# Kernel optimization log

Hardware: AMD Instinct MI355X
Metric: run time of the kernel (lower is better)

## Reference

```python
import jax, jax.numpy as jnp
import numpy as np

N_HEADS = 16
ROPE_BASE = 10000.0


def _rope_tables(T, Dh, dtype):
    # inv_freq over even indices of head_dim, per RotaryEmbedding
    inv_freq = 1.0 / (ROPE_BASE ** (jnp.arange(0, Dh, 2, dtype=jnp.float32) / Dh))
    freqs = jnp.outer(jnp.arange(T, dtype=jnp.float32), inv_freq)  # [T, Dh/2]
    emb = jnp.concatenate([freqs, freqs], axis=-1)                  # [T, Dh]
    return emb.astype(dtype).reshape(1, 1, T, Dh), None


def _rotate_half(x):
    x1, x2 = jnp.split(x, 2, axis=-1)
    return jnp.concatenate([-x2, x1], axis=-1)


def setup_inputs() -> dict:
    key = jax.random.key(0)
    k1, k2, k3 = jax.random.split(key, 3)
    B, T, C = 2, 2048, 1024
    x = jax.random.normal(k1, (B, T, C), dtype=jnp.float32)
    w_qkv = jax.random.normal(k2, (C, 3 * C), dtype=jnp.float32) * (1.0 / np.sqrt(C))
    w_out = jax.random.normal(k3, (C, C), dtype=jnp.float32) * (1.0 / np.sqrt(C))
    return {"x": x, "w_qkv": w_qkv, "w_out": w_out}


def reference(x, w_qkv, w_out):
    B, T, C = x.shape
    H = N_HEADS
    Dh = C // H
    qkv = x @ w_qkv                                   # [B, T, 3C]
    q, k, v = jnp.split(qkv, 3, axis=-1)
    # [B, T, C] -> [B, H, T, Dh]
    def to_heads(t):
        return t.reshape(B, T, H, Dh).transpose(0, 2, 1, 3)
    q, k, v = to_heads(q), to_heads(k), to_heads(v)

    # RoPE
    emb, _ = _rope_tables(T, Dh, x.dtype)             # [1,1,T,Dh] angle table
    cos, sin = jnp.cos(emb), jnp.sin(emb)
    q = q * cos + _rotate_half(q) * sin
    k = k * cos + _rotate_half(k) * sin

    # causal SDPA (eval mode -> no dropout)
    scale = 1.0 / jnp.sqrt(jnp.asarray(Dh, dtype=x.dtype))
    scores = jnp.einsum('bhqd,bhkd->bhqk', q, k) * scale
    causal_mask = jnp.tril(jnp.ones((T, T), dtype=bool))
    scores = jnp.where(causal_mask, scores, jnp.asarray(-jnp.inf, dtype=scores.dtype))
    attn = jax.nn.softmax(scores, axis=-1)
    out = jnp.einsum('bhqk,bhkd->bhqd', attn, v)      # [B,H,T,Dh]
    out = out.transpose(0, 2, 1, 3).reshape(B, T, C)
    return out @ w_out
```

## Files before the change

kernel.cpp:

```cpp
#include <hip/hip_runtime.h>
#include <stdint.h>


typedef __attribute__((ext_vector_type(8))) __bf16 bf16x8;
typedef __attribute__((ext_vector_type(4))) __bf16 bf16x4;
typedef __attribute__((ext_vector_type(4))) float f32x4;

#define MFMA16(a, b, c) __builtin_amdgcn_mfma_f32_16x16x32_bf16((a), (b), (c), 0, 0, 0)

#define SWAIT_VM0()                                     \
    do {                                                \
        asm volatile("s_waitcnt vmcnt(0)" ::: "memory");\
        __builtin_amdgcn_sched_barrier(0);              \
    } while (0)
#define SWAIT_LGKM0()                                     \
    do {                                                  \
        asm volatile("s_waitcnt lgkmcnt(0)" ::: "memory");\
        __builtin_amdgcn_sched_barrier(0);                \
    } while (0)

__device__ __forceinline__ void gl_lds16(const void* g, void* l) {
    __builtin_amdgcn_global_load_lds(
        (const __attribute__((address_space(1))) void*)g,
        (__attribute__((address_space(3))) void*)l, 16, 0, 0);
}

__device__ __forceinline__ unsigned short f2bf(float f) {
    union { float f; unsigned u; } x; x.f = f;
    unsigned r = x.u + 0x7FFFu + ((x.u >> 16) & 1u);
    return (unsigned short)(r >> 16);
}
__device__ __forceinline__ float bf2f(unsigned short h) {
    union { unsigned u; float f; } x; x.u = ((unsigned)h) << 16;
    return x.f;
}
__device__ __forceinline__ f32x4 fmax4(f32x4 a, f32x4 b) {
    f32x4 r;
#pragma unroll
    for (int i = 0; i < 4; i++) r[i] = fmaxf(a[i], b[i]);
    return r;
}

__global__ void cast_f32_bf16(const float* __restrict__ src,
                              unsigned short* __restrict__ dst, int n4) {
    int i = blockIdx.x * 256 + threadIdx.x;
    if (i >= n4) return;
    float4 v = ((const float4*)src)[i];
    ushort4 o;
    o.x = f2bf(v.x); o.y = f2bf(v.y); o.z = f2bf(v.z); o.w = f2bf(v.w);
    ((ushort4*)dst)[i] = o;
}

__global__ void transpose_cast(const float* __restrict__ src,
                               unsigned short* __restrict__ dst, int K, int N) {
    __shared__ float tile[32][33];
    int n0 = blockIdx.x * 32, k0 = blockIdx.y * 32;
    int r = threadIdx.x >> 5, c = threadIdx.x & 31;
#pragma unroll
    for (int i = 0; i < 4; i++) {
        int kk = r + i * 8;
        tile[kk][c] = src[(size_t)(k0 + kk) * N + n0 + c];
    }
    __syncthreads();
#pragma unroll
    for (int i = 0; i < 4; i++) {
        int nn = r + i * 8;
        dst[(size_t)(n0 + nn) * K + k0 + c] = f2bf(tile[c][nn]);
    }
}

__global__ void rope_tables(float2* __restrict__ cst) {
    int idx = blockIdx.x * 256 + threadIdx.x;
    int t = idx >> 5, d = idx & 31;
    float inv = powf(10000.0f, -(float)(2 * d) / 64.0f);
    float a = (float)t * inv;
    cst[idx] = make_float2(cosf(a), sinf(a));
}

template <int MODE>
__global__ __launch_bounds__(256) void gemm_bt(
    const unsigned short* __restrict__ A,
    const unsigned short* __restrict__ Bt,
    unsigned short* __restrict__ oq,
    unsigned short* __restrict__ ok,
    unsigned short* __restrict__ ovt,
    float* __restrict__ of,
    const float2* __restrict__ cst,
    int M_, int N_, int K_) {
    __shared__ __attribute__((aligned(16))) unsigned short ldsA[128 * 64];
    __shared__ __attribute__((aligned(16))) unsigned short ldsB[128 * 64];
    const int tid = threadIdx.x;
    const int lane = tid & 63, wv = tid >> 6;
    const int wr = wv >> 1, wc = wv & 1;
    const int l15 = lane & 15, lg = lane >> 4;
    const int lrow = lane >> 3, lch = lane & 7;
    const int swz = (lch * 16) ^ (lrow << 4);
    const int m0 = blockIdx.x * 128, n0 = blockIdx.y * 128;
    const char* Ab = (const char*)A;
    const char* Bb = (const char*)Bt;
    const size_t rstride = (size_t)K_ * 2;

    f32x4 acc[4][4] = {};

    const int nkt = K_ >> 6;
    for (int kt = 0; kt < nkt; kt++) {
        if (kt) __syncthreads();
#pragma unroll
        for (int ii = 0; ii < 4; ii++) {
            int r0 = wv * 32 + ii * 8;
            gl_lds16(Ab + (size_t)(m0 + r0 + lrow) * rstride + kt * 128 + swz,
                     (char*)ldsA + r0 * 128);
            gl_lds16(Bb + (size_t)(n0 + r0 + lrow) * rstride + kt * 128 + swz,
                     (char*)ldsB + r0 * 128);
        }
        __syncthreads();
#pragma unroll
        for (int ks = 0; ks < 2; ks++) {
            const int kb = ks * 64 + lg * 16;
            bf16x8 af[4], bfr[4];
#pragma unroll
            for (int mf = 0; mf < 4; mf++) {
                int row = wr * 64 + mf * 16 + l15;
                af[mf] = *(const bf16x8*)((const char*)ldsA + row * 128 +
                                          (kb ^ ((row & 7) << 4)));
            }
#pragma unroll
            for (int nf = 0; nf < 4; nf++) {
                int row = wc * 64 + nf * 16 + l15;
                bfr[nf] = *(const bf16x8*)((const char*)ldsB + row * 128 +
                                           (kb ^ ((row & 7) << 4)));
            }
#pragma unroll
            for (int mf = 0; mf < 4; mf++)
#pragma unroll
                for (int nf = 0; nf < 4; nf++)
                    acc[mf][nf] = MFMA16(af[mf], bfr[nf], acc[mf][nf]);
        }
    }

    if (MODE == 0) {
        const int sblk = n0 >> 10;
        if (sblk == 2) {
#pragma unroll
            for (int mf = 0; mf < 4; mf++)
#pragma unroll
                for (int nf = 0; nf < 4; nf++)
#pragma unroll
                    for (int j = 0; j < 4; j++) {
                        int grow = m0 + wr * 64 + mf * 16 + lg * 4 + j;
                        int gcol = n0 + wc * 64 + nf * 16 + l15;
                        int b = grow >> 11, t = grow & 2047;
                        int c = gcol & 1023;
                        int h = c >> 6, d = c & 63;
                        int hb = b * 16 + h;
                        ovt[((size_t)hb * 64 + d) * 2048 + t] =
                            f2bf(acc[mf][nf][j]);
                    }
        } else {
            const float QSC = 0.125f * 1.44269504f;
            unsigned short* dst = (sblk == 0) ? oq : ok;
#pragma unroll
            for (int mf = 0; mf < 4; mf++)
#pragma unroll
                for (int j = 0; j < 4; j++) {
                    int grow = m0 + wr * 64 + mf * 16 + lg * 4 + j;
                    int b = grow >> 11, t = grow & 2047;
#pragma unroll
                    for (int nf = 0; nf < 2; nf++) {
                        int gcol = n0 + wc * 64 + nf * 16 + l15;
                        int c = gcol & 1023;
                        int h = c >> 6;
                        int d = nf * 16 + l15;
                        int hb = b * 16 + h;
                        float2 csv = cst[t * 32 + d];
                        float x1 = acc[mf][nf][j];
                        float x2 = acc[mf][nf + 2][j];
                        float r1 = x1 * csv.x - x2 * csv.y;
                        float r2 = x2 * csv.x + x1 * csv.y;
                        if (sblk == 0) { r1 *= QSC; r2 *= QSC; }
                        size_t base = ((size_t)hb * 2048 + t) * 64;
                        dst[base + d] = f2bf(r1);
                        dst[base + d + 32] = f2bf(r2);
                    }
                }
        }
    } else {
#pragma unroll
        for (int mf = 0; mf < 4; mf++)
#pragma unroll
            for (int nf = 0; nf < 4; nf++)
#pragma unroll
                for (int j = 0; j < 4; j++) {
                    int grow = m0 + wr * 64 + mf * 16 + lg * 4 + j;
                    int gcol = n0 + wc * 64 + nf * 16 + l15;
                    of[(size_t)grow * N_ + gcol] = acc[mf][nf][j];
                }
    }
}

__global__ __launch_bounds__(256) void attn_fwd(
    const unsigned short* __restrict__ Q,
    const unsigned short* __restrict__ K,
    const unsigned short* __restrict__ Vt,
    unsigned short* __restrict__ O) {
    __shared__ __attribute__((aligned(16))) char ldsKV[4][16384];
    __shared__ __attribute__((aligned(16))) char ldsP[4][2560];
    __shared__ float ml[4][32][2];
    const int tid = threadIdx.x, lane = tid & 63, wv = tid >> 6;
    const int l15 = lane & 15, lg = lane >> 4;
    const int lrow = lane >> 3, lch = lane & 7;
    const int swz = (lch * 16) ^ (lrow << 4);

    const int wg = blockIdx.x;
    const int jt = 63 - (wg >> 5);
    const int bh = (wg & 7) * 4 + ((wg >> 3) & 3);
    const int q0 = jt * 32;
    const int nkt = (jt >> 1) + 1;
    const int lo = (wv * nkt) >> 2;
    const int hi = ((wv + 1) * nkt) >> 2;
    const int b = bh >> 4, h = bh & 15;

    const unsigned short* Qh = Q + (size_t)bh * 2048 * 64;
    const char* Kg = (const char*)(K + (size_t)bh * 2048 * 64);
    const char* Vg = (const char*)(Vt + (size_t)bh * 64 * 2048);
    char* Kb = ldsKV[wv];
    char* Vb = ldsKV[wv] + 8192;
    char* Pb = ldsP[wv];

    bf16x8 qa[2][2];
#pragma unroll
    for (int mf = 0; mf < 2; mf++)
#pragma unroll
        for (int ks = 0; ks < 2; ks++)
            qa[mf][ks] = *(const bf16x8*)(Qh + (size_t)(q0 + mf * 16 + l15) * 64 +
                                          ks * 32 + lg * 8);

    auto stage = [&](int k0) {
        const char* kg = Kg + (size_t)k0 * 128;
        const char* vg = Vg + (size_t)k0 * 2;
#pragma unroll
        for (int ii = 0; ii < 8; ii++) {
            gl_lds16(kg + (ii * 8 + lrow) * 128 + swz, Kb + ii * 1024);
            gl_lds16(vg + (size_t)(ii * 8 + lrow) * 4096 + swz, Vb + ii * 1024);
        }
    };

    f32x4 oacc[2][4] = {};
    float mi[2] = {-1e30f, -1e30f}, li[2] = {0.f, 0.f};

    if (lo < hi) {
        stage(lo * 64);
        for (int kt = lo; kt < hi; kt++) {
            const int k0 = kt * 64;
            SWAIT_VM0();
            bf16x8 kb[2][4], vb[2][4];
#pragma unroll
            for (int ks = 0; ks < 2; ks++)
#pragma unroll
                for (int nf = 0; nf < 4; nf++) {
                    int row = nf * 16 + l15;
                    kb[ks][nf] = *(const bf16x8*)(
                        Kb + row * 128 + ((ks * 64 + lg * 16) ^ ((row & 7) << 4)));
                }
#pragma unroll
            for (int ks = 0; ks < 2; ks++)
#pragma unroll
                for (int df = 0; df < 4; df++) {
                    int row = df * 16 + l15;
                    vb[ks][df] = *(const bf16x8*)(
                        Vb + row * 128 + ((ks * 64 + lg * 16) ^ ((row & 7) << 4)));
                }
            f32x4 s[2][4] = {};
#pragma unroll
            for (int ks = 0; ks < 2; ks++)
#pragma unroll
                for (int mf = 0; mf < 2; mf++)
#pragma unroll
                    for (int nf = 0; nf < 4; nf++)
                        s[mf][nf] = MFMA16(kb[ks][nf], qa[mf][ks], s[mf][nf]);
            SWAIT_LGKM0();
            if (kt + 1 < hi) stage(k0 + 64);
            const bool maskt = (kt == nkt - 1);
#pragma unroll
            for (int mf = 0; mf < 2; mf++) {
                if (maskt) {
                    int qrow = q0 + mf * 16 + l15;
#pragma unroll
                    for (int nf = 0; nf < 4; nf++)
#pragma unroll
                        for (int j = 0; j < 4; j++)
                            if (k0 + nf * 16 + lg * 4 + j > qrow)
                                s[mf][nf][j] = -1e30f;
                }
                f32x4 t01 = fmax4(s[mf][0], s[mf][1]);
                f32x4 t23 = fmax4(s[mf][2], s[mf][3]);
                f32x4 tm = fmax4(t01, t23);
                float rmax = fmaxf(fmaxf(tm[0], tm[1]), fmaxf(tm[2], tm[3]));
                rmax = fmaxf(rmax, __shfl_xor(rmax, 16));
                rmax = fmaxf(rmax, __shfl_xor(rmax, 32));
                const float mnew = fmaxf(mi[mf], rmax);
                const float alpha = exp2f(mi[mf] - mnew);
                mi[mf] = mnew;
                float rsum = 0.f;
#pragma unroll
                for (int nf = 0; nf < 4; nf++)
#pragma unroll
                    for (int j = 0; j < 4; j++) {
                        float p = exp2f(s[mf][nf][j] - mnew);
                        s[mf][nf][j] = p;
                        rsum += p;
                    }
                rsum += __shfl_xor(rsum, 16);
                rsum += __shfl_xor(rsum, 32);
                li[mf] = li[mf] * alpha + rsum;
#pragma unroll
                for (int j = 0; j < 4; j++) {
                    float aj = __shfl(alpha, lg * 4 + j);
#pragma unroll
                    for (int df = 0; df < 4; df++) oacc[mf][df][j] *= aj;
                }
            }
#pragma unroll
            for (int ksh = 0; ksh < 2; ksh++) {
#pragma unroll
                for (int mf = 0; mf < 2; mf++) {
                    int row = mf * 16 + l15;
#pragma unroll
                    for (int nf2 = 0; nf2 < 2; nf2++) {
                        bf16x4 pk;
#pragma unroll
                        for (int j = 0; j < 4; j++)
                            pk[j] = (__bf16)s[mf][ksh * 2 + nf2][j];
                        *(bf16x4*)(Pb + row * 80 + nf2 * 32 + lg * 8) = pk;
                    }
                }
                bf16x8 pa[2];
#pragma unroll
                for (int mf = 0; mf < 2; mf++) {
                    int row = mf * 16 + l15;
                    pa[mf] = *(const bf16x8*)(Pb + row * 80 + lg * 16);
                }
#pragma unroll
                for (int mf = 0; mf < 2; mf++)
#pragma unroll
                    for (int df = 0; df < 4; df++)
                        oacc[mf][df] = MFMA16(pa[mf], vb[ksh][df], oacc[mf][df]);
            }
        }
    }

    float* part = (float*)ldsKV[wv];
#pragma unroll
    for (int mf = 0; mf < 2; mf++)
#pragma unroll
        for (int df = 0; df < 4; df++)
#pragma unroll
            for (int j = 0; j < 4; j++)
                part[(mf * 16 + lg * 4 + j) * 68 + df * 16 + l15] =
                    oacc[mf][df][j];
    if (lg == 0) {
#pragma unroll
        for (int mf = 0; mf < 2; mf++) {
            ml[wv][mf * 16 + l15][0] = mi[mf];
            ml[wv][mf * 16 + l15][1] = li[mf];
        }
    }
    __syncthreads();
#pragma unroll
    for (int rr = 0; rr < 8; rr++) {
        const int row = wv * 8 + rr;
        float m01 = fmaxf(ml[0][row][0], ml[1][row][0]);
        float m23 = fmaxf(ml[2][row][0], ml[3][row][0]);
        float m = fmaxf(m01, m23);
        float ssum = 0.f, ov = 0.f;
#pragma unroll
        for (int v = 0; v < 4; v++) {
            float sv = exp2f(ml[v][row][0] - m);
            ssum += ml[v][row][1] * sv;
            ov += ((const float*)ldsKV[v])[row * 68 + lane] * sv;
        }
        O[((size_t)(b * 2048 + q0 + row)) * 1024 + h * 64 + lane] =
            f2bf(ov / ssum);
    }
}

extern "C" void kernel_launch(void* const* d_in, const int* in_sizes, int n_in,
                              void* d_out, int out_size, void* d_ws, size_t ws_size,
                              hipStream_t stream) {
    const float* x     = (const float*)d_in[0];
    const float* w_qkv = (const float*)d_in[1];
    const float* w_out = (const float*)d_in[2];
    float* out = (float*)d_out;
    char* ws = (char*)d_ws;
    const size_t MB = 1024 * 1024;

    unsigned short* xb    = (unsigned short*)(ws);
    unsigned short* wqkvt = (unsigned short*)(ws + 8 * MB);
    unsigned short* woutt = (unsigned short*)(ws + 14 * MB);
    unsigned short* qh    = (unsigned short*)(ws + 16 * MB);
    unsigned short* kh    = (unsigned short*)(ws + 24 * MB);
    unsigned short* vt    = (unsigned short*)(ws + 32 * MB);
    unsigned short* ao    = (unsigned short*)(ws + 40 * MB);
    float2* cst = (float2*)(ws + 48 * MB);

    cast_f32_bf16<<<4096, 256, 0, stream>>>(x, xb, (4096 * 1024) / 4);
    transpose_cast<<<dim3(96, 32), 256, 0, stream>>>(w_qkv, wqkvt, 1024, 3072);
    transpose_cast<<<dim3(32, 32), 256, 0, stream>>>(w_out, woutt, 1024, 1024);
    rope_tables<<<256, 256, 0, stream>>>(cst);

    gemm_bt<0><<<dim3(32, 24), 256, 0, stream>>>(xb, wqkvt, qh, kh, vt, nullptr,
                                                 cst, 4096, 3072, 1024);
    attn_fwd<<<2048, 256, 0, stream>>>(qh, kh, vt, ao);
    gemm_bt<1><<<dim3(32, 8), 256, 0, stream>>>(ao, woutt, nullptr, nullptr,
                                                nullptr, out, nullptr,
                                                4096, 1024, 1024);
}
```

Measured before the change: 139.7 us.

## Shrink attention KV tile to 32 keys and vectorize V-transpose stores

The attention kernel now processes 32-key tiles instead of 64, halving per-wave LDS staging (32KB total for KV) with a new V swizzle layout, and updates the causal tile count and split across waves to match. This finer granularity reduces wasted work on the diagonal tile, balances the per-wave key split better and cuts LDS use, which may allow more workgroups per CU. The cost is twice as many loop iterations, each carrying softmax rescale and sync overhead. Separately, the QKV GEMM epilogue writes the transposed V as packed 4-element bf16 vectors instead of scalar stores.

Result: slower. 148.2 us (+6.1%).

```diff
diff --git a/kernel.cpp b/kernel.cpp
--- a/kernel.cpp
+++ b/kernel.cpp
@@ -144,18 +144,18 @@
 #pragma unroll
             for (int mf = 0; mf < 4; mf++)
 #pragma unroll
-                for (int nf = 0; nf < 4; nf++)
-#pragma unroll
-                    for (int j = 0; j < 4; j++) {
-                        int grow = m0 + wr * 64 + mf * 16 + lg * 4 + j;
-                        int gcol = n0 + wc * 64 + nf * 16 + l15;
-                        int b = grow >> 11, t = grow & 2047;
-                        int c = gcol & 1023;
-                        int h = c >> 6, d = c & 63;
-                        int hb = b * 16 + h;
-                        ovt[((size_t)hb * 64 + d) * 2048 + t] =
-                            f2bf(acc[mf][nf][j]);
-                    }
+                for (int nf = 0; nf < 4; nf++) {
+                    int grow = m0 + wr * 64 + mf * 16 + lg * 4;
+                    int gcol = n0 + wc * 64 + nf * 16 + l15;
+                    int b = grow >> 11, t = grow & 2047;
+                    int c = gcol & 1023;
+                    int h = c >> 6, d = c & 63;
+                    int hb = b * 16 + h;
+                    bf16x4 pk;
+#pragma unroll
+                    for (int j = 0; j < 4; j++) pk[j] = (__bf16)acc[mf][nf][j];
+                    *(bf16x4*)(ovt + ((size_t)hb * 64 + d) * 2048 + t) = pk;
+                }
         } else {
             const float QSC = 0.125f * 1.44269504f;
             unsigned short* dst = (sblk == 0) ? oq : ok;
@@ -203,19 +203,21 @@
     const unsigned short* __restrict__ K,
     const unsigned short* __restrict__ Vt,
     unsigned short* __restrict__ O) {
-    __shared__ __attribute__((aligned(16))) char ldsKV[4][16384];
+    __shared__ __attribute__((aligned(16))) char ldsKV[4][8192];
     __shared__ __attribute__((aligned(16))) char ldsP[4][2560];
     __shared__ float ml[4][32][2];
     const int tid = threadIdx.x, lane = tid & 63, wv = tid >> 6;
     const int l15 = lane & 15, lg = lane >> 4;
     const int lrow = lane >> 3, lch = lane & 7;
-    const int swz = (lch * 16) ^ (lrow << 4);
+    const int swzK = (lch * 16) ^ (lrow << 4);
+    const int vrow = lane >> 2;
+    const int vcs = (((lane & 3) ^ (vrow & 3)) * 16);
 
     const int wg = blockIdx.x;
     const int jt = 63 - (wg >> 5);
     const int bh = (wg & 7) * 4 + ((wg >> 3) & 3);
     const int q0 = jt * 32;
-    const int nkt = (jt >> 1) + 1;
+    const int nkt = jt + 1;
     const int lo = (wv * nkt) >> 2;
     const int hi = ((wv + 1) * nkt) >> 2;
     const int b = bh >> 4, h = bh & 15;
@@ -224,7 +226,7 @@
     const char* Kg = (const char*)(K + (size_t)bh * 2048 * 64);
     const char* Vg = (const char*)(Vt + (size_t)bh * 64 * 2048);
     char* Kb = ldsKV[wv];
-    char* Vb = ldsKV[wv] + 8192;
+    char* Vb = ldsKV[wv] + 4096;
     char* Pb = ldsP[wv];
 
     bf16x8 qa[2][2];
@@ -239,9 +241,12 @@
         const char* kg = Kg + (size_t)k0 * 128;
         const char* vg = Vg + (size_t)k0 * 2;
 #pragma unroll
-        for (int ii = 0; ii < 8; ii++) {
-            gl_lds16(kg + (ii * 8 + lrow) * 128 + swz, Kb + ii * 1024);
-            gl_lds16(vg + (size_t)(ii * 8 + lrow) * 4096 + swz, Vb + ii * 1024);
+        for (int ii = 0; ii < 4; ii++)
+            gl_lds16(kg + (ii * 8 + lrow) * 128 + swzK, Kb + ii * 1024);
+#pragma unroll
+        for (int ii = 0; ii < 4; ii++) {
+            int row = ii * 16 + vrow;
+            gl_lds16(vg + (size_t)row * 4096 + vcs, Vb + ii * 1024);
         }
     };
 
@@ -249,52 +254,48 @@
     float mi[2] = {-1e30f, -1e30f}, li[2] = {0.f, 0.f};
 
     if (lo < hi) {
-        stage(lo * 64);
+        stage(lo * 32);
         for (int kt = lo; kt < hi; kt++) {
-            const int k0 = kt * 64;
+            const int k0 = kt * 32;
             SWAIT_VM0();
-            bf16x8 kb[2][4], vb[2][4];
+            bf16x8 kb[2][2], vb[4];
 #pragma unroll
             for (int ks = 0; ks < 2; ks++)
 #pragma unroll
-                for (int nf = 0; nf < 4; nf++) {
+                for (int nf = 0; nf < 2; nf++) {
                     int row = nf * 16 + l15;
                     kb[ks][nf] = *(const bf16x8*)(
                         Kb + row * 128 + ((ks * 64 + lg * 16) ^ ((row & 7) << 4)));
                 }
 #pragma unroll
+            for (int df = 0; df < 4; df++) {
+                int row = df * 16 + l15;
+                vb[df] = *(const bf16x8*)(
+                    Vb + row * 64 + ((lg ^ (row & 3)) * 16));
+            }
+            f32x4 s[2][2] = {};
+#pragma unroll
             for (int ks = 0; ks < 2; ks++)
 #pragma unroll
-                for (int df = 0; df < 4; df++) {
-                    int row = df * 16 + l15;
-                    vb[ks][df] = *(const bf16x8*)(
-                        Vb + row * 128 + ((ks * 64 + lg * 16) ^ ((row & 7) << 4)));
-                }
-            f32x4 s[2][4] = {};
-#pragma unroll
-            for (int ks = 0; ks < 2; ks++)
-#pragma unroll
                 for (int mf = 0; mf < 2; mf++)
 #pragma unroll
-                    for (int nf = 0; nf < 4; nf++)
+                    for (int nf = 0; nf < 2; nf++)
                         s[mf][nf] = MFMA16(kb[ks][nf], qa[mf][ks], s[mf][nf]);
             SWAIT_LGKM0();
-            if (kt + 1 < hi) stage(k0 + 64);
+            if (kt + 1 < hi) stage(k0 + 32);
             const bool maskt = (kt == nkt - 1);
 #pragma unroll
             for (int mf = 0; mf < 2; mf++) {
                 if (maskt) {
                     int qrow = q0 + mf * 16 + l15;
 #pragma unroll
-                    for (int nf = 0; nf < 4; nf++)
+                    for (int nf = 0; nf < 2; nf++)
 #pragma unroll
                         for (int j = 0; j < 4; j++)
                             if (k0 + nf * 16 + lg * 4 + j > qrow)
                                 s[mf][nf][j] = -1e30f;
                 }
-                f32x4 t01 = fmax4(s[mf][0], s[mf][1]);
-                f32x4 t23 = fmax4(s[mf][2], s[mf][3]);
-                f32x4 tm = fmax4(t01, t23);
+                f32x4 tm = fmax4(s[mf][0], s[mf][1]);
                 float rmax = fmaxf(fmaxf(tm[0], tm[1]), fmaxf(tm[2], tm[3]));
                 rmax = fmaxf(rmax, __shfl_xor(rmax, 16));
                 rmax = fmaxf(rmax, __shfl_xor(rmax, 32));
@@ -303,7 +304,7 @@
                 mi[mf] = mnew;
                 float rsum = 0.f;
 #pragma unroll
-                for (int nf = 0; nf < 4; nf++)
+                for (int nf = 0; nf < 2; nf++)
 #pragma unroll
                     for (int j = 0; j < 4; j++) {
                         float p = exp2f(s[mf][nf][j] - mnew);
@@ -319,21 +320,16 @@
 #pragma unroll
                     for (int df = 0; df < 4; df++) oacc[mf][df][j] *= aj;
                 }
+#pragma unroll
+                for (int nf = 0; nf < 2; nf++) {
+                    bf16x4 pk;
+#pragma unroll
+                    for (int j = 0; j < 4; j++) pk[j] = (__bf16)s[mf][nf][j];
+                    int row = mf * 16 + l15;
+                    *(bf16x4*)(Pb + row * 80 + nf * 32 + lg * 8) = pk;
+                }
             }
-#pragma unroll
-            for (int ksh = 0; ksh < 2; ksh++) {
-#pragma unroll
-                for (int mf = 0; mf < 2; mf++) {
-                    int row = mf * 16 + l15;
-#pragma unroll
-                    for (int nf2 = 0; nf2 < 2; nf2++) {
-                        bf16x4 pk;
-#pragma unroll
-                        for (int j = 0; j < 4; j++)
-                            pk[j] = (__bf16)s[mf][ksh * 2 + nf2][j];
-                        *(bf16x4*)(Pb + row * 80 + nf2 * 32 + lg * 8) = pk;
-                    }
-                }
+            {
                 bf16x8 pa[2];
 #pragma unroll
                 for (int mf = 0; mf < 2; mf++) {
@@ -344,7 +340,7 @@
                 for (int mf = 0; mf < 2; mf++)
 #pragma unroll
                     for (int df = 0; df < 4; df++)
-                        oacc[mf][df] = MFMA16(pa[mf], vb[ksh][df], oacc[mf][df]);
+                        oacc[mf][df] = MFMA16(pa[mf], vb[df], oacc[mf][df]);
             }
         }
     }
@@ -356,7 +352,7 @@
         for (int df = 0; df < 4; df++)
 #pragma unroll
             for (int j = 0; j < 4; j++)
-                part[(mf * 16 + lg * 4 + j) * 68 + df * 16 + l15] =
+                part[(mf * 16 + lg * 4 + j) * 64 + df * 16 + l15] =
                     oacc[mf][df][j];
     if (lg == 0) {
 #pragma unroll
@@ -377,7 +373,7 @@
         for (int v = 0; v < 4; v++) {
             float sv = exp2f(ml[v][row][0] - m);
             ssum += ml[v][row][1] * sv;
-            ov += ((const float*)ldsKV[v])[row * 68 + lane] * sv;
+            ov += ((const float*)ldsKV[v])[row * 64 + lane] * sv;
         }
         O[((size_t)(b * 2048 + q0 + row)) * 1024 + h * 64 + lane] =
             f2bf(ov / ssum);
```
